# Kernel tuning notes

Measured on AMD Instinct MI355X. Metric: run time of the kernel, lower is better.

## Reference

```python
import jax, jax.numpy as jnp
import numpy as np

D, H, COND, MLP_RATIO = 1024, 16, 1024, 4
HD = D // H
DFF = MLP_RATIO * D


def layer_norm(x, w, eps=1e-5):
    xf = x.astype(jnp.float32)
    mu = jnp.mean(xf, axis=-1, keepdims=True)
    var = jnp.mean((xf - mu) ** 2, axis=-1, keepdims=True)
    return (xf - mu) * jax.lax.rsqrt(var + eps) * w


def rms_norm(x, w, eps=1e-6):
    xf = x.astype(jnp.float32)
    rms = jnp.sqrt(jnp.mean(xf * xf, axis=-1, keepdims=True) + eps)
    return (xf / rms * w).astype(x.dtype)


def rotate_half(x):
    x1, x2 = x[..., : x.shape[-1] // 2], x[..., x.shape[-1] // 2:]
    return jnp.concatenate([-x2, x1], axis=-1)


def apply_rope(x, cos, sin):
    return x * cos + rotate_half(x) * sin


def setup_inputs() -> dict:
    key = jax.random.key(0)
    ks = jax.random.split(key, 16)
    B, S = 4, 2048
    pos = jnp.arange(S, dtype=jnp.float32)
    inv = 1.0 / (10000.0 ** (jnp.arange(0, HD, 2, dtype=jnp.float32) / HD))
    freqs = pos[:, None] * inv[None, :]              # (S, HD/2)
    emb = jnp.concatenate([freqs, freqs], axis=-1)   # (S, HD)
    return {
        "x": jax.random.normal(ks[0], (B, S, D), jnp.float32),
        "cos": jnp.cos(emb)[None, :, None, :],        # (1,S,1,HD)
        "sin": jnp.sin(emb)[None, :, None, :],
        "c": jax.random.normal(ks[1], (B, COND), jnp.float32),
        "norm1_w": jnp.ones((D,), jnp.float32),
        "Wqkv": jax.random.normal(ks[2], (D, 3 * D), jnp.float32) * 0.02,
        "Wout": jax.random.normal(ks[3], (D, D), jnp.float32) * 0.02,
        "q_norm_w": jnp.ones((HD,), jnp.float32),
        "k_norm_w": jnp.ones((HD,), jnp.float32),
        "norm2_w": jnp.ones((D,), jnp.float32),
        "W1": jax.random.normal(ks[4], (D, DFF), jnp.float32) * 0.02,
        "b1": jnp.zeros((DFF,), jnp.float32),
        "W2": jax.random.normal(ks[5], (DFF, D), jnp.float32) * 0.02,
        "b2": jnp.zeros((D,), jnp.float32),
        "ada_W": jax.random.normal(ks[6], (COND, 6 * D), jnp.float32) * 0.02,
        "ada_b": jnp.zeros((6 * D,), jnp.float32),
    }


def reference(x, cos, sin, c, norm1_w, Wqkv, Wout, q_norm_w, k_norm_w,
              norm2_w, W1, b1, W2, b2, ada_W, ada_b):
    B, S, _ = x.shape
    mod = (c @ ada_W + ada_b)[:, None, :]            # (B,1,6D)
    sh_msa, sc_msa, g_msa, sh_mlp, sc_mlp, g_mlp = jnp.split(mod, 6, axis=-1)

    x_norm = layer_norm(x, norm1_w) * (1 + sc_msa) + sh_msa
    qkv = (x_norm @ Wqkv).reshape(B, S, 3, H, HD)
    q, k, v = qkv[:, :, 0], qkv[:, :, 1], qkv[:, :, 2]  # (B,S,H,HD)
    q = apply_rope(rms_norm(q, q_norm_w), cos, sin)
    k = apply_rope(rms_norm(k, k_norm_w), cos, sin)

    scale = 1.0 / jnp.sqrt(jnp.float32(HD))
    logits = jnp.einsum('bqhd,bkhd->bhqk', q, k) * scale
    probs = jax.nn.softmax(logits, axis=-1)
    attn = jnp.einsum('bhqk,bkhd->bqhd', probs, v).reshape(B, S, D)

    x = x + g_msa * (attn @ Wout)

    x_norm = layer_norm(x, norm2_w) * (1 + sc_mlp) + sh_mlp
    h = jax.nn.gelu(x_norm @ W1 + b1, approximate=True)
    x = x + g_mlp * (h @ W2 + b2)
    return x
```

## Files before the change

kernel.cpp:

```cpp
#include <hip/hip_runtime.h>
#include <hip/hip_bf16.h>
#include <math.h>

typedef __bf16 bf16;
typedef __bf16 bf16x8 __attribute__((ext_vector_type(8)));
typedef __bf16 bf16x4 __attribute__((ext_vector_type(4)));
typedef float f32x4 __attribute__((ext_vector_type(4)));
typedef short s16x4 __attribute__((ext_vector_type(4)));

#define S_LEN 2048
#define NTOK 8192
#define DIM 1024
#define NH 16
#define HEADD 64
#define DFF 4096
#define MODD 6144

__device__ __forceinline__ float gelu_fast(float x) {
  float u = 0.7978845608028654f * (x + 0.044715f * x * x * x);
  float e = __builtin_amdgcn_exp2f(-2.8853900817779268f * u);
  return x * __builtin_amdgcn_rcpf(1.0f + e);
}

__device__ __forceinline__ void gl_lds16(const bf16* g, bf16* l) {
  __builtin_amdgcn_global_load_lds(
      (const __attribute__((address_space(1))) unsigned int*)g,
      (__attribute__((address_space(3))) unsigned int*)l, 16, 0, 0);
}

__global__ __launch_bounds__(256) void init_mod_kernel(
    const float* __restrict__ ada_b, float* __restrict__ mod) {
  int i = blockIdx.x * 256 + threadIdx.x;
  mod[i] = ada_b[i % MODD];
}

__global__ __launch_bounds__(256) void ada_gemm_kernel(
    const float* __restrict__ cnd, const float* __restrict__ W,
    float* __restrict__ mod) {
  int n = blockIdx.x * 256 + threadIdx.x;
  int k0 = blockIdx.y * 128;
  float a0 = 0.f, a1 = 0.f, a2 = 0.f, a3 = 0.f;
  for (int k = k0; k < k0 + 128; ++k) {
    float w = W[(size_t)k * MODD + n];
    a0 = fmaf(cnd[k], w, a0);
    a1 = fmaf(cnd[1024 + k], w, a1);
    a2 = fmaf(cnd[2048 + k], w, a2);
    a3 = fmaf(cnd[3072 + k], w, a3);
  }
  atomicAdd(&mod[n], a0);
  atomicAdd(&mod[MODD + n], a1);
  atomicAdd(&mod[2 * MODD + n], a2);
  atomicAdd(&mod[3 * MODD + n], a3);
}

__global__ __launch_bounds__(256) void transpose_cast_kernel(
    const float* __restrict__ W, bf16* __restrict__ Wt, int K, int N) {
  __shared__ float tile[32][33];
  int n0 = blockIdx.x * 32, k0 = blockIdx.y * 32;
  int r = threadIdx.x >> 3;
  int c4 = (threadIdx.x & 7) * 4;
  float4 v = *(const float4*)&W[(size_t)(k0 + r) * N + n0 + c4];
  tile[r][c4 + 0] = v.x; tile[r][c4 + 1] = v.y;
  tile[r][c4 + 2] = v.z; tile[r][c4 + 3] = v.w;
  __syncthreads();
  bf16x4 o;
  o[0] = (bf16)tile[c4 + 0][r];
  o[1] = (bf16)tile[c4 + 1][r];
  o[2] = (bf16)tile[c4 + 2][r];
  o[3] = (bf16)tile[c4 + 3][r];
  *(bf16x4*)&Wt[(size_t)(n0 + r) * K + k0 + c4] = o;
}

__global__ __launch_bounds__(256) void vtrans_kernel(
    const bf16* __restrict__ qkv, bf16* __restrict__ VT) {
  __shared__ __align__(16) bf16 t[64][72];
  const int bh = blockIdx.y;
  const int b = bh >> 4, h = bh & 15;
  const int s0 = blockIdx.x * 64;
  const int tid = threadIdx.x;
  {
    const int r = tid >> 2;
    const int c = (tid & 3) * 16;
    const bf16* src =
        qkv + (size_t)(b * S_LEN + s0 + r) * 3072 + 2048 + h * 64 + c;
    *(bf16x8*)&t[r][c] = *(const bf16x8*)src;
    *(bf16x8*)&t[r][c + 8] = *(const bf16x8*)(src + 8);
  }
  __syncthreads();
  {
    const int d = tid & 63;
    const int sc = (tid >> 6) * 16;
    bf16x8 o0, o1;
#pragma unroll
    for (int j = 0; j < 8; ++j) o0[j] = t[sc + j][d];
#pragma unroll
    for (int j = 0; j < 8; ++j) o1[j] = t[sc + 8 + j][d];
    bf16* dst = VT + (size_t)(bh * 64 + d) * S_LEN + s0 + sc;
    *(bf16x8*)dst = o0;
    *(bf16x8*)(dst + 8) = o1;
  }
}

__global__ __launch_bounds__(256) void ln_mod_kernel(
    const float* __restrict__ x, const float* __restrict__ w,
    const float* __restrict__ mod, int sh_off, int sc_off,
    bf16* __restrict__ out) {
  __shared__ float red[8];
  const int row = blockIdx.x;
  const int b = row >> 11;
  const int tid = threadIdx.x;
  const float4 v = ((const float4*)(x + (size_t)row * DIM))[tid];
  float s1 = v.x + v.y + v.z + v.w;
  float s2 = v.x * v.x + v.y * v.y + v.z * v.z + v.w * v.w;
  for (int off = 32; off > 0; off >>= 1) {
    s1 += __shfl_down(s1, off, 64);
    s2 += __shfl_down(s2, off, 64);
  }
  const int wid = tid >> 6;
  if ((tid & 63) == 0) { red[wid] = s1; red[4 + wid] = s2; }
  __syncthreads();
  s1 = red[0] + red[1] + red[2] + red[3];
  s2 = red[4] + red[5] + red[6] + red[7];
  const float mu = s1 * (1.0f / DIM);
  const float inv = rsqrtf(s2 * (1.0f / DIM) - mu * mu + 1e-5f);
  const int c = tid * 4;
  const float* mb = mod + (size_t)b * MODD;
  float xs[4] = {v.x, v.y, v.z, v.w};
  bf16x4 o;
#pragma unroll
  for (int j = 0; j < 4; ++j)
    o[j] = (bf16)(((xs[j] - mu) * inv) * w[c + j] * (1.0f + mb[sc_off + c + j]) +
                  mb[sh_off + c + j]);
  *(bf16x4*)(out + (size_t)row * DIM + c) = o;
}

template <int EPI, int MT, int BN>
__global__ __launch_bounds__(256) void gemm_bt(
    const bf16* __restrict__ A, const bf16* __restrict__ Bt,
    bf16* __restrict__ Cb, float* __restrict__ Cf,
    const float* __restrict__ bias, const float* __restrict__ gmod,
    const float* __restrict__ resid, const float* __restrict__ cosb,
    const float* __restrict__ sinb, const float* __restrict__ qw,
    const float* __restrict__ kw, int M, int N, int K) {
  constexpr int IM = MT / 32;
  constexpr int JN = BN / 32;
  constexpr int AG = MT / 64;
  constexpr int BG = BN / 64;
  __shared__ __align__(16) bf16 As[2][MT * 32];
  __shared__ __align__(16) bf16 Bs[2][BN * 32];
  const int tid = threadIdx.x;
  const int wid = tid >> 6;
  const int lane = tid & 63;
  const int l15 = lane & 15;
  const int quad = lane >> 4;
  const int m0 = blockIdx.y * MT;
  const int n0 = blockIdx.x * BN;
  const int wm = (wid & 1) * (MT / 2);
  const int wn = (wid >> 1) * (BN / 2);

  const int srow = wid * 16 + (lane >> 2);
  const int scol = (lane & 3) * 8;
  const bf16* Ap = A + (size_t)(m0 + srow) * K + scol;
  const bf16* Bp = Bt + (size_t)(n0 + srow) * K + scol;

#pragma unroll
  for (int g = 0; g < AG; ++g)
    gl_lds16(Ap + (size_t)g * 64 * K, As[0] + g * 2048 + wid * 512);
#pragma unroll
  for (int g = 0; g < BG; ++g)
    gl_lds16(Bp + (size_t)g * 64 * K, Bs[0] + g * 2048 + wid * 512);
  __syncthreads();

  f32x4 acc[IM][JN] = {};
  int cur = 0;

  for (int kt = 0; kt < K; kt += 32) {
    if (kt + 32 < K) {
      const int nxt = cur ^ 1;
#pragma unroll
      for (int g = 0; g < AG; ++g)
        gl_lds16(Ap + (size_t)g * 64 * K + kt + 32,
                 As[nxt] + g * 2048 + wid * 512);
#pragma unroll
      for (int g = 0; g < BG; ++g)
        gl_lds16(Bp + (size_t)g * 64 * K + kt + 32,
                 Bs[nxt] + g * 2048 + wid * 512);
    }

    bf16x8 af[IM], bfr[JN];
#pragma unroll
    for (int i = 0; i < IM; ++i)
      af[i] = *(const bf16x8*)&As[cur][(wm + i * 16 + l15) * 32 + quad * 8];
#pragma unroll
    for (int j = 0; j < JN; ++j)
      bfr[j] = *(const bf16x8*)&Bs[cur][(wn + j * 16 + l15) * 32 + quad * 8];
#pragma unroll
    for (int i = 0; i < IM; ++i)
#pragma unroll
      for (int j = 0; j < JN; ++j)
        acc[i][j] = __builtin_amdgcn_mfma_f32_16x16x32_bf16(af[i], bfr[j],
                                                            acc[i][j], 0, 0, 0);

    __syncthreads();
    cur ^= 1;
  }

  if (EPI == 4 && n0 < 2048) {
    const float* nw = ((n0 + wn) < 1024) ? qw : kw;
    float wv[4];
#pragma unroll
    for (int j = 0; j < 4; ++j) wv[j] = nw[j * 16 + l15];
#pragma unroll
    for (int i = 0; i < IM; ++i) {
#pragma unroll
      for (int r = 0; r < 4; ++r) {
        const int m = m0 + wm + i * 16 + quad * 4 + r;
        const int s = m & (S_LEN - 1);
        float v[4];
        float ss = 0.f;
#pragma unroll
        for (int j = 0; j < 4; ++j) { v[j] = acc[i][j][r]; ss += v[j] * v[j]; }
        ss += __shfl_xor(ss, 1, 64);
        ss += __shfl_xor(ss, 2, 64);
        ss += __shfl_xor(ss, 4, 64);
        ss += __shfl_xor(ss, 8, 64);
        const float inv = rsqrtf(ss * (1.0f / HEADD) + 1e-6f);
        float xn[4];
#pragma unroll
        for (int j = 0; j < 4; ++j) xn[j] = v[j] * inv * wv[j];
#pragma unroll
        for (int j = 0; j < 4; ++j) {
          const int d = j * 16 + l15;
          const float rot = (j < 2) ? -xn[j + 2] : xn[j - 2];
          const float o = xn[j] * cosb[s * HEADD + d] + rot * sinb[s * HEADD + d];
          Cb[(size_t)m * N + n0 + wn + d] = (bf16)o;
        }
      }
    }
    return;
  }

#pragma unroll
  for (int i = 0; i < IM; ++i) {
#pragma unroll
    for (int r = 0; r < 4; ++r) {
      const int m = m0 + wm + i * 16 + quad * 4 + r;
#pragma unroll
      for (int j = 0; j < JN; ++j) {
        const int n = n0 + wn + j * 16 + l15;
        float v = acc[i][j][r];
        if (EPI == 0 || EPI == 4) {
          Cb[(size_t)m * N + n] = (bf16)v;
        } else if (EPI == 1) {
          const int b = m >> 11;
          Cf[(size_t)m * N + n] =
              resid[(size_t)m * N + n] + gmod[(size_t)b * MODD + n] * v;
        } else if (EPI == 2) {
          v += bias[n];
          Cb[(size_t)m * N + n] = (bf16)gelu_fast(v);
        } else {
          v += bias[n];
          const int b = m >> 11;
          Cf[(size_t)m * N + n] =
              resid[(size_t)m * N + n] + gmod[(size_t)b * MODD + n] * v;
        }
      }
    }
  }
}

__global__ __launch_bounds__(256) void attn_kernel(
    const bf16* __restrict__ qkv, const bf16* __restrict__ VT,
    bf16* __restrict__ Opart, float* __restrict__ psumbuf) {
  __shared__ __align__(16) bf16 Ks[4096];
  __shared__ __align__(16) bf16 Vs[4096];
  const int bh = blockIdx.y;
  const int b = bh >> 4;
  const int h = bh & 15;
  const int q0 = blockIdx.x * 128;
  const int split = blockIdx.z;
  const int tid = threadIdx.x;
  const int wid = tid >> 6;
  const int lane = tid & 63;
  const int l15 = lane & 15;
  const int quad = lane >> 4;

  bf16x8 aq[2][2];
#pragma unroll
  for (int i = 0; i < 2; ++i) {
    const int qrow = q0 + wid * 32 + i * 16 + l15;
    const size_t qbase = (size_t)(b * S_LEN + qrow) * (3 * DIM) + h * HEADD;
    aq[i][0] = *(const bf16x8*)(qkv + qbase + quad * 8);
    aq[i][1] = *(const bf16x8*)(qkv + qbase + 32 + quad * 8);
  }

  const int rstage = lane;
  const int rsw = rstage & 7;
  const bf16* krow =
      qkv + (size_t)(b * S_LEN + split * 1024 + rstage) * 3072 + DIM + h * HEADD;
  const bf16* vrow = VT + (size_t)(bh * 64 + rstage) * S_LEN + split * 1024;

  bf16x8 kreg[2], vreg[2];
#pragma unroll
  for (int rr = 0; rr < 2; ++rr) {
    const int ck = wid + 4 * rr;
    kreg[rr] = *(const bf16x8*)(krow + ck * 8);
    vreg[rr] = *(const bf16x8*)(vrow + ck * 8);
  }

  const float cexp = 0.125f * 1.44269504f;
  f32x4 oacc[2][4] = {};
  float psum[2] = {0.f, 0.f};

  for (int t = 0; t < 16; ++t) {
    __syncthreads();
#pragma unroll
    for (int rr = 0; rr < 2; ++rr) {
      const int ck = wid + 4 * rr;
      const int sw = ((ck ^ rsw) << 3);
      *(bf16x8*)&Ks[rstage * 64 + sw] = kreg[rr];
      *(bf16x8*)&Vs[rstage * 64 + sw] = vreg[rr];
    }
    __syncthreads();
    if (t < 15) {
      krow += 64 * 3072;
      vrow += 64;
#pragma unroll
      for (int rr = 0; rr < 2; ++rr) {
        const int ck = wid + 4 * rr;
        kreg[rr] = *(const bf16x8*)(krow + ck * 8);
        vreg[rr] = *(const bf16x8*)(vrow + ck * 8);
      }
    }

    f32x4 sc[2][4] = {};
#pragma unroll
    for (int hh = 0; hh < 2; ++hh) {
#pragma unroll
      for (int cc = 0; cc < 4; ++cc) {
        const int row = cc * 16 + l15;
        const bf16x8 kf =
            *(const bf16x8*)&Ks[row * 64 + (((quad + 4 * hh) ^ (l15 & 7)) << 3)];
#pragma unroll
        for (int i = 0; i < 2; ++i)
          sc[i][cc] = __builtin_amdgcn_mfma_f32_16x16x32_bf16(kf, aq[i][hh],
                                                              sc[i][cc], 0, 0, 0);
      }
    }

    s16x4 pf[2][4];
#pragma unroll
    for (int i = 0; i < 2; ++i)
#pragma unroll
      for (int cc = 0; cc < 4; ++cc) {
        bf16x4 pb;
#pragma unroll
        for (int r = 0; r < 4; ++r) {
          const float p = __builtin_amdgcn_exp2f(fmaf(sc[i][cc][r], cexp, -8.0f));
          psum[i] += p;
          pb[r] = (bf16)p;
        }
        pf[i][cc] = __builtin_bit_cast(s16x4, pb);
      }

#pragma unroll
    for (int j = 0; j < 4; ++j) {
      const int d = 16 * j + l15;
      const int drow = d * 64;
      const int dsw = d & 7;
#pragma unroll
      for (int cc = 0; cc < 4; ++cc) {
        const int ck = 2 * cc + (quad >> 1);
        const s16x4 vf =
            *(const s16x4*)&Vs[drow + ((ck ^ dsw) << 3) + ((quad & 1) << 2)];
#pragma unroll
        for (int i = 0; i < 2; ++i)
          oacc[i][j] = __builtin_amdgcn_mfma_f32_16x16x16bf16_1k(pf[i][cc], vf,
                                                                 oacc[i][j], 0, 0, 0);
      }
    }
  }

#pragma unroll
  for (int i = 0; i < 2; ++i) {
    float ps = psum[i];
    ps += __shfl_xor(ps, 16, 64);
    ps += __shfl_xor(ps, 32, 64);
    if (lane < 16) {
      const int qrow = q0 + wid * 32 + i * 16 + lane;
      psumbuf[(size_t)split * (NTOK * NH) + (size_t)(b * S_LEN + qrow) * NH + h] = ps;
    }
#pragma unroll
    for (int r = 0; r < 4; ++r) {
      const int m = q0 + wid * 32 + i * 16 + quad * 4 + r;
#pragma unroll
      for (int j = 0; j < 4; ++j)
        Opart[(size_t)split * (NTOK * DIM) +
              ((size_t)(b * S_LEN + m) * NH + h) * HEADD + j * 16 + l15] =
            (bf16)oacc[i][j][r];
    }
  }
}

__global__ __launch_bounds__(256) void attn_reduce_kernel(
    const bf16* __restrict__ Opart, const float* __restrict__ psumbuf,
    bf16* __restrict__ attn) {
  const int g = blockIdx.x * 256 + threadIdx.x;
  const int token = g >> 7;
  const int rem = g & 127;
  const int h = rem >> 3;
  const int d0 = (rem & 7) * 8;
  const size_t off = ((size_t)token * NH + h) * HEADD + d0;
  const bf16x8 o0 = *(const bf16x8*)(Opart + off);
  const bf16x8 o1 = *(const bf16x8*)(Opart + (size_t)NTOK * DIM + off);
  const float l = psumbuf[token * NH + h] + psumbuf[NTOK * NH + token * NH + h];
  const float invl = 1.0f / l;
  bf16x8 o;
#pragma unroll
  for (int j = 0; j < 8; ++j)
    o[j] = (bf16)(((float)o0[j] + (float)o1[j]) * invl);
  *(bf16x8*)(attn + off) = o;
}

extern "C" void kernel_launch(void* const* d_in, const int* in_sizes, int n_in,
                              void* d_out, int out_size, void* d_ws,
                              size_t ws_size, hipStream_t stream) {
  const float* x = (const float*)d_in[0];
  const float* cosb = (const float*)d_in[1];
  const float* sinb = (const float*)d_in[2];
  const float* cnd = (const float*)d_in[3];
  const float* norm1_w = (const float*)d_in[4];
  const float* Wqkv = (const float*)d_in[5];
  const float* Wout = (const float*)d_in[6];
  const float* q_norm_w = (const float*)d_in[7];
  const float* k_norm_w = (const float*)d_in[8];
  const float* norm2_w = (const float*)d_in[9];
  const float* W1 = (const float*)d_in[10];
  const float* b1 = (const float*)d_in[11];
  const float* W2 = (const float*)d_in[12];
  const float* b2 = (const float*)d_in[13];
  const float* ada_W = (const float*)d_in[14];
  const float* ada_b = (const float*)d_in[15];
  float* out = (float*)d_out;

  char* p = (char*)d_ws;
  float* mod = (float*)p;   p += (size_t)4 * MODD * 4;
  bf16* WqkvT = (bf16*)p;   p += (size_t)3072 * 1024 * 2;
  bf16* WoutT = (bf16*)p;   p += (size_t)1024 * 1024 * 2;
  bf16* W1T = (bf16*)p;     p += (size_t)4096 * 1024 * 2;
  bf16* W2T = (bf16*)p;     p += (size_t)1024 * 4096 * 2;
  bf16* XN = (bf16*)p;      p += (size_t)NTOK * DIM * 2;
  bf16* QKV = (bf16*)p;     p += (size_t)NTOK * 3 * DIM * 2;
  bf16* ATTN = (bf16*)p;    p += (size_t)NTOK * DIM * 2;
  bf16* Hbuf = (bf16*)p;    p += (size_t)NTOK * DFF * 2;
  bf16* VT = Hbuf;
  bf16* Opart = Hbuf + (size_t)NTOK * DIM;
  float* psumbuf = (float*)(Hbuf + (size_t)3 * NTOK * DIM);

  init_mod_kernel<<<96, 256, 0, stream>>>(ada_b, mod);
  ada_gemm_kernel<<<dim3(24, 8), 256, 0, stream>>>(cnd, ada_W, mod);
  transpose_cast_kernel<<<dim3(96, 32), 256, 0, stream>>>(Wqkv, WqkvT, 1024, 3072);
  transpose_cast_kernel<<<dim3(32, 32), 256, 0, stream>>>(Wout, WoutT, 1024, 1024);
  transpose_cast_kernel<<<dim3(128, 32), 256, 0, stream>>>(W1, W1T, 1024, 4096);
  transpose_cast_kernel<<<dim3(32, 128), 256, 0, stream>>>(W2, W2T, 4096, 1024);
  ln_mod_kernel<<<NTOK, 256, 0, stream>>>(x, norm1_w, mod, 0, 1024, XN);
  gemm_bt<4, 128, 128><<<dim3(24, 64), 256, 0, stream>>>(
      XN, WqkvT, QKV, nullptr, nullptr, nullptr, nullptr, cosb, sinb,
      q_norm_w, k_norm_w, NTOK, 3072, 1024);
  vtrans_kernel<<<dim3(32, 64), 256, 0, stream>>>(QKV, VT);
  attn_kernel<<<dim3(16, 64, 2), 256, 0, stream>>>(QKV, VT, Opart, psumbuf);
  attn_reduce_kernel<<<4096, 256, 0, stream>>>(Opart, psumbuf, ATTN);
  gemm_bt<1, 128, 128><<<dim3(8, 64), 256, 0, stream>>>(
      ATTN, WoutT, nullptr, out, nullptr, mod + 2 * 1024, x, nullptr, nullptr,
      nullptr, nullptr, NTOK, 1024, 1024);
  ln_mod_kernel<<<NTOK, 256, 0, stream>>>(out, norm2_w, mod, 3 * 1024, 4 * 1024, XN);
  gemm_bt<2, 128, 128><<<dim3(32, 64), 256, 0, stream>>>(
      XN, W1T, Hbuf, nullptr, b1, nullptr, nullptr, nullptr, nullptr,
      nullptr, nullptr, NTOK, DFF, 1024);
  gemm_bt<3, 128, 128><<<dim3(8, 64), 256, 0, stream>>>(
      Hbuf, W2T, nullptr, out, b2, mod + 5 * 1024, out, nullptr, nullptr,
      nullptr, nullptr, NTOK, 1024, DFF);
  (void)in_sizes; (void)n_in; (void)out_size; (void)ws_size;
}
```

Measured before the change: 618.2 us.

## Use 16x16x32 MFMA for PV, MFMA row sums, XCD-aware block mapping

Restructures the attention inner loop so the P·V product uses the wider 16x16x32 bf16 MFMA. K rows are permuted in LDS so that the score layout lines up with 8-element P fragments. Softmax row sums are now computed by an MFMA against a ones vector instead of scalar adds and shuffles. Block indices are remapped so consecutive blocks sharing a (batch, head, split) land on the same XCD for L2 reuse, and s_setprio is raised around the MFMA sections. This adds complexity to the LDS row permutation and relies on the grid shape matching the hardcoded remap.

```diff
diff --git a/kernel.cpp b/kernel.cpp
--- a/kernel.cpp
+++ b/kernel.cpp
@@ -274,11 +274,16 @@
     bf16* __restrict__ Opart, float* __restrict__ psumbuf) {
   __shared__ __align__(16) bf16 Ks[4096];
   __shared__ __align__(16) bf16 Vs[4096];
-  const int bh = blockIdx.y;
+  const int flat = blockIdx.x + 16 * (blockIdx.y + 64 * blockIdx.z);
+  const int xcd = flat & 7;
+  const int idx = flat >> 3;
+  const int pair = xcd * 16 + (idx >> 4);
+  const int qblk = idx & 15;
+  const int bh = pair >> 1;
+  const int split = pair & 1;
   const int b = bh >> 4;
   const int h = bh & 15;
-  const int q0 = blockIdx.x * 128;
-  const int split = blockIdx.z;
+  const int q0 = qblk * 128;
   const int tid = threadIdx.x;
   const int wid = tid >> 6;
   const int lane = tid & 63;
@@ -294,11 +299,12 @@
     aq[i][1] = *(const bf16x8*)(qkv + qbase + 32 + quad * 8);
   }
 
-  const int rstage = lane;
-  const int rsw = rstage & 7;
+  const int ksrow = (lane & 32) | ((lane & 4) << 2) | ((lane & 24) >> 1) | (lane & 3);
+  const int ksw = ksrow & 7;
+  const int vsw = lane & 7;
   const bf16* krow =
-      qkv + (size_t)(b * S_LEN + split * 1024 + rstage) * 3072 + DIM + h * HEADD;
-  const bf16* vrow = VT + (size_t)(bh * 64 + rstage) * S_LEN + split * 1024;
+      qkv + (size_t)(b * S_LEN + split * 1024 + lane) * 3072 + DIM + h * HEADD;
+  const bf16* vrow = VT + (size_t)(bh * 64 + lane) * S_LEN + split * 1024;
 
   bf16x8 kreg[2], vreg[2];
 #pragma unroll
@@ -309,17 +315,18 @@
   }
 
   const float cexp = 0.125f * 1.44269504f;
+  const bf16 one = (bf16)1.0f;
+  const bf16x8 ones8 = {one, one, one, one, one, one, one, one};
   f32x4 oacc[2][4] = {};
-  float psum[2] = {0.f, 0.f};
+  f32x4 psacc[2] = {};
 
   for (int t = 0; t < 16; ++t) {
     __syncthreads();
 #pragma unroll
     for (int rr = 0; rr < 2; ++rr) {
       const int ck = wid + 4 * rr;
-      const int sw = ((ck ^ rsw) << 3);
-      *(bf16x8*)&Ks[rstage * 64 + sw] = kreg[rr];
-      *(bf16x8*)&Vs[rstage * 64 + sw] = vreg[rr];
+      *(bf16x8*)&Ks[ksrow * 64 + ((ck ^ ksw) << 3)] = kreg[rr];
+      *(bf16x8*)&Vs[lane * 64 + ((ck ^ vsw) << 3)] = vreg[rr];
     }
     __syncthreads();
     if (t < 15) {
@@ -334,6 +341,7 @@
     }
 
     f32x4 sc[2][4] = {};
+    __builtin_amdgcn_s_setprio(1);
 #pragma unroll
     for (int hh = 0; hh < 2; ++hh) {
 #pragma unroll
@@ -347,48 +355,57 @@
                                                               sc[i][cc], 0, 0, 0);
       }
     }
-
-    s16x4 pf[2][4];
+    __builtin_amdgcn_s_setprio(0);
+
+    bf16x8 pf[2][2];
 #pragma unroll
     for (int i = 0; i < 2; ++i)
 #pragma unroll
-      for (int cc = 0; cc < 4; ++cc) {
-        bf16x4 pb;
-#pragma unroll
-        for (int r = 0; r < 4; ++r) {
-          const float p = __builtin_amdgcn_exp2f(fmaf(sc[i][cc][r], cexp, -8.0f));
-          psum[i] += p;
-          pb[r] = (bf16)p;
+      for (int c2 = 0; c2 < 2; ++c2) {
+        bf16x8 pb;
+#pragma unroll
+        for (int j = 0; j < 8; ++j) {
+          const float p = __builtin_amdgcn_exp2f(
+              fmaf(sc[i][2 * c2 + (j >> 2)][j & 3], cexp, -8.0f));
+          pb[j] = (bf16)p;
         }
-        pf[i][cc] = __builtin_bit_cast(s16x4, pb);
-      }
-
+        pf[i][c2] = pb;
+      }
+
+    __builtin_amdgcn_s_setprio(1);
+#pragma unroll
+    for (int i = 0; i < 2; ++i)
+#pragma unroll
+      for (int c2 = 0; c2 < 2; ++c2)
+        psacc[i] = __builtin_amdgcn_mfma_f32_16x16x32_bf16(pf[i][c2], ones8,
+                                                           psacc[i], 0, 0, 0);
 #pragma unroll
     for (int j = 0; j < 4; ++j) {
       const int d = 16 * j + l15;
       const int drow = d * 64;
       const int dsw = d & 7;
 #pragma unroll
-      for (int cc = 0; cc < 4; ++cc) {
-        const int ck = 2 * cc + (quad >> 1);
-        const s16x4 vf =
-            *(const s16x4*)&Vs[drow + ((ck ^ dsw) << 3) + ((quad & 1) << 2)];
+      for (int c2 = 0; c2 < 2; ++c2) {
+        const bf16x8 vf =
+            *(const bf16x8*)&Vs[drow + (((c2 * 4 + quad) ^ dsw) << 3)];
 #pragma unroll
         for (int i = 0; i < 2; ++i)
-          oacc[i][j] = __builtin_amdgcn_mfma_f32_16x16x16bf16_1k(pf[i][cc], vf,
-                                                                 oacc[i][j], 0, 0, 0);
-      }
-    }
+          oacc[i][j] = __builtin_amdgcn_mfma_f32_16x16x32_bf16(pf[i][c2], vf,
+                                                               oacc[i][j], 0, 0, 0);
+      }
+    }
+    __builtin_amdgcn_s_setprio(0);
   }
 
 #pragma unroll
   for (int i = 0; i < 2; ++i) {
-    float ps = psum[i];
-    ps += __shfl_xor(ps, 16, 64);
-    ps += __shfl_xor(ps, 32, 64);
-    if (lane < 16) {
-      const int qrow = q0 + wid * 32 + i * 16 + lane;
-      psumbuf[(size_t)split * (NTOK * NH) + (size_t)(b * S_LEN + qrow) * NH + h] = ps;
+    if (l15 == 0) {
+#pragma unroll
+      for (int r = 0; r < 4; ++r) {
+        const int qrow = q0 + wid * 32 + i * 16 + quad * 4 + r;
+        psumbuf[(size_t)split * (NTOK * NH) +
+                (size_t)(b * S_LEN + qrow) * NH + h] = psacc[i][r];
+      }
     }
 #pragma unroll
     for (int r = 0; r < 4; ++r) {
```

After: 618.2 us. Within noise of the previous version (-0.0%).
